# Performance work log

Hardware: AMD Instinct MI355X
Metric: run time of the kernel (lower is better)

## Reference

```python
import jax, jax.numpy as jnp
import numpy as np

B, T, C = 256, 256, 147
BPM, H_DIM, NH = 32, 64, 4
HD = H_DIM // NH


def setup_inputs() -> dict:
    key = jax.random.key(0)
    ks = jax.random.split(key, 12)
    def lin(k, fan_in, fan_out):
        bound = 1.0 / np.sqrt(fan_in)
        kw, kb = jax.random.split(k)
        W = jax.random.uniform(kw, (fan_in, fan_out), jnp.float32, -bound, bound)
        b = jax.random.uniform(kb, (fan_out,), jnp.float32, -bound, bound)
        return W, b
    Wq, bq = lin(ks[0], C, H_DIM)
    Wk, bk = lin(ks[1], C, H_DIM)
    Wv, bv = lin(ks[2], C, H_DIM)
    Wb, bb = lin(ks[3], BPM, H_DIM)
    Wo, bo = lin(ks[4], H_DIM, C)
    pose = jax.random.normal(ks[5], (B, T, C), jnp.float32)
    bpm_emb = jax.random.normal(ks[6], (B, BPM), jnp.float32)
    return {"pose": pose, "bpm_emb": bpm_emb,
            "Wq": Wq, "bq": bq, "Wk": Wk, "bk": bk, "Wv": Wv, "bv": bv,
            "Wb": Wb, "bb": bb, "Wo": Wo, "bo": bo}


def reference(pose, bpm_emb, Wq, bq, Wk, bk, Wv, bv, Wb, bb, Wo, bo):
    Bb, Tt, Cc = pose.shape
    scale = HD ** -0.5
    # projections -> [B, H, T, hd]
    def split_heads(x):
        return x.reshape(Bb, Tt, NH, HD).transpose(0, 2, 1, 3)
    q = split_heads(pose @ Wq + bq)
    k = split_heads(pose @ Wk + bk)
    v = split_heads(pose @ Wv + bv)
    # bpm-conditioned key bias: [B, H, 1, hd]
    bpm_feat = (bpm_emb @ Wb + bb).reshape(Bb, 1, NH, HD).transpose(0, 2, 1, 3)
    k = k + bpm_feat
    # attention
    scores = jnp.einsum('bhqd,bhkd->bhqk', q, k) * scale
    attn = jax.nn.softmax(scores, axis=-1)
    out = jnp.einsum('bhqk,bhkd->bhqd', attn, v)
    out = out.transpose(0, 2, 1, 3).reshape(Bb, Tt, NH * HD)
    return out @ Wo + bo
```

## Files before the change

### kernel.cpp

```cpp
#include <hip/hip_runtime.h>

constexpr int kC = 147, kH = 64, kBPM = 32;

typedef __attribute__((ext_vector_type(8)))  short bf16x8;
typedef __attribute__((ext_vector_type(4)))  float f32x4;
typedef __attribute__((ext_vector_type(16))) float f32x16;
typedef __attribute__((ext_vector_type(2)))  unsigned u32x2;
typedef __attribute__((ext_vector_type(4)))  unsigned u32x4;

__device__ __forceinline__ short f2bf(float f) {
    unsigned u = __builtin_bit_cast(unsigned, f);
    u += 0x7fffu + ((u >> 16) & 1u);
    return (short)(u >> 16);
}
__device__ __forceinline__ unsigned cvt_pk(float lo, float hi) {
    unsigned r;
    asm("v_cvt_pk_bf16_f32 %0, %1, %2" : "=v"(r) : "v"(lo), "v"(hi));
    return r;
}
#define MFMA16(a,b,c) __builtin_amdgcn_mfma_f32_16x16x32_bf16((a),(b),(c),0,0,0)
#define MFMA32(a,b,c) __builtin_amdgcn_mfma_f32_32x32x16_bf16((a),(b),(c),0,0,0)

#if __has_builtin(__builtin_amdgcn_exp2f)
  #define EXP2(x) __builtin_amdgcn_exp2f(x)
#else
  #define EXP2(x) __expf((x) * 0.6931471805599453f)
#endif
constexpr float kQScale = 0.25f * 1.4426950408889634f;

constexpr int QS  = 72;
constexpr int VS  = 264;
constexpr int WSS = 168;
constexpr int WOS = 72;

__device__ __forceinline__ void stage_w_regs(const float* wr ,
                                             short* Ws, int tid) {
    #pragma unroll
    for (int it = 0; it < 5; ++it) {
        const int i = it * 1024 + tid;
        const int c = i & 63, k = (i >> 6) * 2;
        *(unsigned*)&Ws[c * WSS + (k ^ (((c >> 3) & 3) << 3))]
            = cvt_pk(wr[2*it], wr[2*it + 1]);
    }
}

__global__ __launch_bounds__(1024, 4) void fused_kernel(
    const float* __restrict__ pose, const float* __restrict__ bpm_emb,
    const float* __restrict__ Wq, const float* __restrict__ bq,
    const float* __restrict__ Wk, const float* __restrict__ bk,
    const float* __restrict__ Wv, const float* __restrict__ bv,
    const float* __restrict__ Wb, const float* __restrict__ bb,
    const float* __restrict__ Wo, const float* __restrict__ bo,
    float* __restrict__ out)
{
    __shared__ __align__(16) short qs[256 * QS];
    __shared__ __align__(16) short ks_[256 * QS];
    __shared__ __align__(16) short vt[kH * VS];
    __shared__ __align__(16) short Ws[11520];
    __shared__ float bias_s[192];

    const int tid = threadIdx.x;
    const int w = tid >> 6, lane = tid & 63;
    const int ll = lane & 15, lq = lane >> 4;
    const int lm = lane & 31, lh = lane >> 5;
    const int b = blockIdx.x;
    const size_t pbase = (size_t)b * 256 * kC;

    float wq_r[10], wk_r[10], wv_r[10], wo_r[10];
    #pragma unroll
    for (int it = 0; it < 5; ++it) {
        const int i = it * 1024 + tid;
        const int c = i & 63, k = (i >> 6) * 2;
        const bool b0 = k < kC, b1 = k + 1 < kC;
        wq_r[2*it]   = b0 ? Wq[k * kH + c] * kQScale : 0.f;
        wq_r[2*it+1] = b1 ? Wq[(k + 1) * kH + c] * kQScale : 0.f;
        wk_r[2*it]   = b0 ? Wk[k * kH + c] : 0.f;
        wk_r[2*it+1] = b1 ? Wk[(k + 1) * kH + c] : 0.f;
        wv_r[2*it]   = b0 ? Wv[k * kH + c] : 0.f;
        wv_r[2*it+1] = b1 ? Wv[(k + 1) * kH + c] : 0.f;
        const int n = i % 160, ko = (i / 160) * 2;
        wo_r[2*it]   = (n < kC) ? Wo[ko * kC + n] : 0.f;
        wo_r[2*it+1] = (n < kC) ? Wo[(ko + 1) * kC + n] : 0.f;
    }

    bf16x8 pf[5];
    {
        const int row = w * 16 + ll;
        const float* prow = pose + pbase + (size_t)row * kC;
        #pragma unroll
        for (int ksp = 0; ksp < 5; ++ksp) {
            const int c0 = ksp * 32 + lq * 8;
            float v[8];
            if (c0 + 8 <= kC) {
                const float4 f0 = *(const float4*)(prow + c0);
                const float4 f1 = *(const float4*)(prow + c0 + 4);
                v[0]=f0.x; v[1]=f0.y; v[2]=f0.z; v[3]=f0.w;
                v[4]=f1.x; v[5]=f1.y; v[6]=f1.z; v[7]=f1.w;
            } else {
                #pragma unroll
                for (int e = 0; e < 8; ++e) v[e] = (c0 + e < kC) ? prow[c0 + e] : 0.f;
            }
            const u32x4 t = { cvt_pk(v[0], v[1]), cvt_pk(v[2], v[3]),
                              cvt_pk(v[4], v[5]), cvt_pk(v[6], v[7]) };
            pf[ksp] = __builtin_bit_cast(bf16x8, t);
        }
    }
    if (tid < 192) {
        const int m = tid >> 6, c = tid & 63;
        float a = ((m == 0) ? bq : (m == 1) ? bk : bv)[c];
        if (m == 1) {
            a += bb[c];
            #pragma unroll
            for (int k2 = 0; k2 < kBPM; ++k2)
                a = fmaf(bpm_emb[b * kBPM + k2], Wb[k2 * kH + c], a);
        }
        if (m == 0) a *= kQScale;
        bias_s[tid] = a;
    }
    stage_w_regs(wq_r, Ws, tid);
    __syncthreads();

    #pragma unroll
    for (int m = 0; m < 3; ++m) {
        f32x4 acc[4];
        #pragma unroll
        for (int mt = 0; mt < 4; ++mt) acc[mt] = (f32x4){0.f,0.f,0.f,0.f};
        #pragma unroll
        for (int ksp = 0; ksp < 5; ++ksp)
            #pragma unroll
            for (int mt = 0; mt < 4; ++mt) {
                const int c = mt * 16 + ll;
                const int key = ((c >> 3) & 3) << 3;
                const bf16x8 wf = *(const bf16x8*)(Ws + c * WSS + ((ksp*32 + lq*8) ^ key));
                acc[mt] = MFMA16(wf, pf[ksp], acc[mt]);
            }
        __syncthreads();
        if (m == 0)      stage_w_regs(wk_r, Ws, tid);
        else if (m == 1) stage_w_regs(wv_r, Ws, tid);
        else {
            #pragma unroll
            for (int it = 0; it < 5; ++it) {
                const int i = it * 1024 + tid;
                const int n = i % 160, k = (i / 160) * 2;
                *(unsigned*)&Ws[n * WOS + (k ^ (((n >> 3) & 3) << 3))]
                    = cvt_pk(wo_r[2*it], wo_r[2*it + 1]);
            }
        }
        const int row = w * 16 + ll;
        #pragma unroll
        for (int mt = 0; mt < 4; ++mt) {
            const int c0 = mt * 16 + 4 * lq;
            const float4 bv4 = *(const float4*)&bias_s[m * kH + c0];
            if (m < 2) {
                const u32x2 pk = { cvt_pk(acc[mt][0] + bv4.x, acc[mt][1] + bv4.y),
                                   cvt_pk(acc[mt][2] + bv4.z, acc[mt][3] + bv4.w) };
                *(u32x2*)((m == 0 ? qs : ks_) + row * QS + c0) = pk;
            } else {
                vt[(c0 + 0) * VS + row] = f2bf(acc[mt][0] + bv4.x);
                vt[(c0 + 1) * VS + row] = f2bf(acc[mt][1] + bv4.y);
                vt[(c0 + 2) * VS + row] = f2bf(acc[mt][2] + bv4.z);
                vt[(c0 + 3) * VS + row] = f2bf(acc[mt][3] + bv4.w);
            }
        }
        __syncthreads();
    }

    const int h = w & 3;
    const int q0 = (w >> 2) * 64;
    bf16x8 qf[2];
    #pragma unroll
    for (int s32 = 0; s32 < 2; ++s32)
        qf[s32] = *(const bf16x8*)(qs + (q0 + s32*32 + lm) * QS + h*16 + lh*8);

    f32x16 oacc[2];
    #pragma unroll
    for (int s32 = 0; s32 < 2; ++s32)
        oacc[s32] = (f32x16){0.f,0.f,0.f,0.f,0.f,0.f,0.f,0.f,
                             0.f,0.f,0.f,0.f,0.f,0.f,0.f,0.f};
    float lp[2] = {0.f, 0.f};
    const int vrow = h * 16 + (lm & 15);
    const f32x16 z16 = {0.f,0.f,0.f,0.f,0.f,0.f,0.f,0.f,
                        0.f,0.f,0.f,0.f,0.f,0.f,0.f,0.f};

    #pragma unroll 2
    for (int jb = 0; jb < 8; ++jb) {
        const int j0 = jb * 32;
        const bf16x8 kf  = *(const bf16x8*)(ks_ + (j0 + lm) * QS + h*16 + lh*8);
        const bf16x8 va0 = *(const bf16x8*)(vt + vrow * VS + j0 + lh*8);
        const bf16x8 va1 = *(const bf16x8*)(vt + vrow * VS + j0 + 16 + lh*8);
        #pragma unroll
        for (int s32 = 0; s32 < 2; ++s32) {
            const f32x16 s = MFMA32(kf, qf[s32], z16);
            float sum = 0.f;
            unsigned u[8];
            #pragma unroll
            for (int g = 0; g < 4; ++g) {
                const float p0 = EXP2(s[4*g + 0]);
                const float p1 = EXP2(s[4*g + 1]);
                const float p2 = EXP2(s[4*g + 2]);
                const float p3 = EXP2(s[4*g + 3]);
                sum += (p0 + p1) + (p2 + p3);
                u[2*g]   = cvt_pk(p0, p1);
                u[2*g+1] = cvt_pk(p2, p3);
            }
            lp[s32] += sum;
            unsigned a0 = u[0], a1 = u[1], b0 = u[2], b1 = u[3];
            asm("v_permlane32_swap_b32 %0, %1" : "+v"(a0), "+v"(b0));
            asm("v_permlane32_swap_b32 %0, %1" : "+v"(a1), "+v"(b1));
            unsigned c0 = u[4], c1 = u[5], d0 = u[6], d1 = u[7];
            asm("v_permlane32_swap_b32 %0, %1" : "+v"(c0), "+v"(d0));
            asm("v_permlane32_swap_b32 %0, %1" : "+v"(c1), "+v"(d1));
            const u32x4 pb0 = { a0, a1, b0, b1 };
            const u32x4 pb1 = { c0, c1, d0, d1 };
            oacc[s32] = MFMA32(va0, __builtin_bit_cast(bf16x8, pb0), oacc[s32]);
            oacc[s32] = MFMA32(va1, __builtin_bit_cast(bf16x8, pb1), oacc[s32]);
        }
    }
    #pragma unroll
    for (int s32 = 0; s32 < 2; ++s32) {
        const float l2 = lp[s32] + __shfl_xor(lp[s32], 32);
        const float inv = 1.f / l2;
        const int row = q0 + s32 * 32 + lm;
        const u32x2 pkA = { cvt_pk(oacc[s32][0] * inv, oacc[s32][1] * inv),
                            cvt_pk(oacc[s32][2] * inv, oacc[s32][3] * inv) };
        *(u32x2*)(qs + row * QS + h*16 + 4*lh) = pkA;
        const u32x2 pkB = { cvt_pk(oacc[s32][4] * inv, oacc[s32][5] * inv),
                            cvt_pk(oacc[s32][6] * inv, oacc[s32][7] * inv) };
        *(u32x2*)(qs + row * QS + h*16 + 8 + 4*lh) = pkB;
    }
    __syncthreads();

    bf16x8 xf[2];
    #pragma unroll
    for (int k2 = 0; k2 < 2; ++k2)
        xf[k2] = *(const bf16x8*)(qs + (w*16 + ll) * QS + k2*32 + lq*8);

    f32x4 po[10];
    #pragma unroll
    for (int mt = 0; mt < 10; ++mt) po[mt] = (f32x4){0.f,0.f,0.f,0.f};
    #pragma unroll
    for (int k2 = 0; k2 < 2; ++k2)
        #pragma unroll
        for (int mt = 0; mt < 10; ++mt) {
            const int n = mt * 16 + ll;
            const int key = ((n >> 3) & 3) << 3;
            const bf16x8 wf = *(const bf16x8*)(Ws + n * WOS + ((k2*32 + lq*8) ^ key));
            po[mt] = MFMA16(wf, xf[k2], po[mt]);
        }
    {
        const int row = w * 16 + ll;
        float* orow = out + ((size_t)b * 256 + row) * kC;
        #pragma unroll
        for (int mt = 0; mt < 10; ++mt) {
            const int c0 = mt * 16 + 4 * lq;
            if (mt < 9) {
                const float4 bv4 = *(const float4*)(bo + c0);
                float4 o;
                o.x = po[mt][0] + bv4.x; o.y = po[mt][1] + bv4.y;
                o.z = po[mt][2] + bv4.z; o.w = po[mt][3] + bv4.w;
                *(float4*)(orow + c0) = o;
            } else {
                #pragma unroll
                for (int r = 0; r < 4; ++r) {
                    const int c = c0 + r;
                    if (c < kC) orow[c] = po[mt][r] + bo[c];
                }
            }
        }
    }
}

extern "C" void kernel_launch(void* const* d_in, const int* in_sizes, int n_in,
                              void* d_out, int out_size, void* d_ws, size_t ws_size,
                              hipStream_t stream) {
    const float* pose    = (const float*)d_in[0];
    const float* bpm_emb = (const float*)d_in[1];
    const float* Wq = (const float*)d_in[2];  const float* bq = (const float*)d_in[3];
    const float* Wk = (const float*)d_in[4];  const float* bk = (const float*)d_in[5];
    const float* Wv = (const float*)d_in[6];  const float* bv = (const float*)d_in[7];
    const float* Wb = (const float*)d_in[8];  const float* bb = (const float*)d_in[9];
    const float* Wo = (const float*)d_in[10]; const float* bo = (const float*)d_in[11];
    float* out = (float*)d_out;

    fused_kernel<<<256, 1024, 0, stream>>>(
        pose, bpm_emb, Wq, bq, Wk, bk, Wv, bv, Wb, bb, Wo, bo, out);
}
```

Measured before the change: 132.0 us.

## Stage Q/K/V weights together, fuse projections, XOR-swizzle unpadded LDS tiles

Stages all three Q/K/V weight matrices into shared memory at once, so the three projections run in one MFMA loop with a single barrier instead of three staged rounds. The Q/K/V tiles drop their padding and use XOR swizzles to avoid bank conflicts. The Wo weight load is deferred until after the projections, which cuts live registers. The attention loop is restructured to process one 32-row query slice at a time, halving the accumulator registers. The cost is more LDS for the concurrently staged weights, which may reduce occupancy, and extra index arithmetic for the swizzles.

```diff
diff --git a/kernel.cpp b/kernel.cpp
--- a/kernel.cpp
+++ b/kernel.cpp
@@ -28,9 +28,7 @@
 #endif
 constexpr float kQScale = 0.25f * 1.4426950408889634f;
 
-constexpr int QS  = 72;
-constexpr int VS  = 264;
-constexpr int WSS = 168;
+constexpr int WSS = 160;
 constexpr int WOS = 72;
 
 __device__ __forceinline__ void stage_w_regs(const float* wr ,
@@ -53,11 +51,15 @@
     const float* __restrict__ Wo, const float* __restrict__ bo,
     float* __restrict__ out)
 {
-    __shared__ __align__(16) short qs[256 * QS];
-    __shared__ __align__(16) short ks_[256 * QS];
-    __shared__ __align__(16) short vt[kH * VS];
-    __shared__ __align__(16) short Ws[11520];
+    __shared__ __align__(16) short Wqkv[3 * 64 * WSS];
+    __shared__ __align__(16) short qs[256 * 64];
+    __shared__ __align__(16) short ks_[256 * 64];
+    __shared__ __align__(16) short vt[64 * 256];
     __shared__ float bias_s[192];
+    short* const Wqs = Wqkv;
+    short* const Wks = Wqkv + 64 * WSS;
+    short* const Wvs = Wqkv + 2 * 64 * WSS;
+    short* const Wos = Wqkv;
 
     const int tid = threadIdx.x;
     const int w = tid >> 6, lane = tid & 63;
@@ -65,23 +67,6 @@
     const int lm = lane & 31, lh = lane >> 5;
     const int b = blockIdx.x;
     const size_t pbase = (size_t)b * 256 * kC;
-
-    float wq_r[10], wk_r[10], wv_r[10], wo_r[10];
-    #pragma unroll
-    for (int it = 0; it < 5; ++it) {
-        const int i = it * 1024 + tid;
-        const int c = i & 63, k = (i >> 6) * 2;
-        const bool b0 = k < kC, b1 = k + 1 < kC;
-        wq_r[2*it]   = b0 ? Wq[k * kH + c] * kQScale : 0.f;
-        wq_r[2*it+1] = b1 ? Wq[(k + 1) * kH + c] * kQScale : 0.f;
-        wk_r[2*it]   = b0 ? Wk[k * kH + c] : 0.f;
-        wk_r[2*it+1] = b1 ? Wk[(k + 1) * kH + c] : 0.f;
-        wv_r[2*it]   = b0 ? Wv[k * kH + c] : 0.f;
-        wv_r[2*it+1] = b1 ? Wv[(k + 1) * kH + c] : 0.f;
-        const int n = i % 160, ko = (i / 160) * 2;
-        wo_r[2*it]   = (n < kC) ? Wo[ko * kC + n] : 0.f;
-        wo_r[2*it+1] = (n < kC) ? Wo[(ko + 1) * kC + n] : 0.f;
-    }
 
     bf16x8 pf[5];
     {
@@ -105,92 +90,115 @@
             pf[ksp] = __builtin_bit_cast(bf16x8, t);
         }
     }
-    if (tid < 192) {
-        const int m = tid >> 6, c = tid & 63;
-        float a = ((m == 0) ? bq : (m == 1) ? bk : bv)[c];
-        if (m == 1) {
-            a += bb[c];
-            #pragma unroll
-            for (int k2 = 0; k2 < kBPM; ++k2)
-                a = fmaf(bpm_emb[b * kBPM + k2], Wb[k2 * kH + c], a);
-        }
-        if (m == 0) a *= kQScale;
-        bias_s[tid] = a;
-    }
-    stage_w_regs(wq_r, Ws, tid);
+    {
+        float wq_r[10], wk_r[10], wv_r[10];
+        #pragma unroll
+        for (int it = 0; it < 5; ++it) {
+            const int i = it * 1024 + tid;
+            const int c = i & 63, k = (i >> 6) * 2;
+            const bool b0 = k < kC, b1 = k + 1 < kC;
+            wq_r[2*it]   = b0 ? Wq[k * kH + c] * kQScale : 0.f;
+            wq_r[2*it+1] = b1 ? Wq[(k + 1) * kH + c] * kQScale : 0.f;
+            wk_r[2*it]   = b0 ? Wk[k * kH + c] : 0.f;
+            wk_r[2*it+1] = b1 ? Wk[(k + 1) * kH + c] : 0.f;
+            wv_r[2*it]   = b0 ? Wv[k * kH + c] : 0.f;
+            wv_r[2*it+1] = b1 ? Wv[(k + 1) * kH + c] : 0.f;
+        }
+        if (tid < 192) {
+            const int m = tid >> 6, c = tid & 63;
+            float a = ((m == 0) ? bq : (m == 1) ? bk : bv)[c];
+            if (m == 1) {
+                a += bb[c];
+                #pragma unroll
+                for (int k2 = 0; k2 < kBPM; ++k2)
+                    a = fmaf(bpm_emb[b * kBPM + k2], Wb[k2 * kH + c], a);
+            }
+            if (m == 0) a *= kQScale;
+            bias_s[tid] = a;
+        }
+        stage_w_regs(wq_r, Wqs, tid);
+        stage_w_regs(wk_r, Wks, tid);
+        stage_w_regs(wv_r, Wvs, tid);
+    }
     __syncthreads();
 
-    #pragma unroll
-    for (int m = 0; m < 3; ++m) {
-        f32x4 acc[4];
-        #pragma unroll
-        for (int mt = 0; mt < 4; ++mt) acc[mt] = (f32x4){0.f,0.f,0.f,0.f};
-        #pragma unroll
-        for (int ksp = 0; ksp < 5; ++ksp)
-            #pragma unroll
-            for (int mt = 0; mt < 4; ++mt) {
-                const int c = mt * 16 + ll;
-                const int key = ((c >> 3) & 3) << 3;
-                const bf16x8 wf = *(const bf16x8*)(Ws + c * WSS + ((ksp*32 + lq*8) ^ key));
-                acc[mt] = MFMA16(wf, pf[ksp], acc[mt]);
-            }
-        __syncthreads();
-        if (m == 0)      stage_w_regs(wk_r, Ws, tid);
-        else if (m == 1) stage_w_regs(wv_r, Ws, tid);
-        else {
-            #pragma unroll
-            for (int it = 0; it < 5; ++it) {
-                const int i = it * 1024 + tid;
-                const int n = i % 160, k = (i / 160) * 2;
-                *(unsigned*)&Ws[n * WOS + (k ^ (((n >> 3) & 3) << 3))]
-                    = cvt_pk(wo_r[2*it], wo_r[2*it + 1]);
-            }
-        }
+    f32x4 aQ[4], aK[4], aV[4];
+    #pragma unroll
+    for (int mt = 0; mt < 4; ++mt) {
+        aQ[mt] = (f32x4){0.f,0.f,0.f,0.f};
+        aK[mt] = (f32x4){0.f,0.f,0.f,0.f};
+        aV[mt] = (f32x4){0.f,0.f,0.f,0.f};
+    }
+    #pragma unroll
+    for (int ksp = 0; ksp < 5; ++ksp)
+        #pragma unroll
+        for (int mt = 0; mt < 4; ++mt) {
+            const int c = mt * 16 + ll;
+            const int ko = (ksp*32 + lq*8) ^ (((c >> 3) & 3) << 3);
+            aQ[mt] = MFMA16(*(const bf16x8*)(Wqs + c * WSS + ko), pf[ksp], aQ[mt]);
+            aK[mt] = MFMA16(*(const bf16x8*)(Wks + c * WSS + ko), pf[ksp], aK[mt]);
+            aV[mt] = MFMA16(*(const bf16x8*)(Wvs + c * WSS + ko), pf[ksp], aV[mt]);
+        }
+    {
         const int row = w * 16 + ll;
+        const int rkey = (ll & 7) << 3;
         #pragma unroll
         for (int mt = 0; mt < 4; ++mt) {
             const int c0 = mt * 16 + 4 * lq;
-            const float4 bv4 = *(const float4*)&bias_s[m * kH + c0];
-            if (m < 2) {
-                const u32x2 pk = { cvt_pk(acc[mt][0] + bv4.x, acc[mt][1] + bv4.y),
-                                   cvt_pk(acc[mt][2] + bv4.z, acc[mt][3] + bv4.w) };
-                *(u32x2*)((m == 0 ? qs : ks_) + row * QS + c0) = pk;
-            } else {
-                vt[(c0 + 0) * VS + row] = f2bf(acc[mt][0] + bv4.x);
-                vt[(c0 + 1) * VS + row] = f2bf(acc[mt][1] + bv4.y);
-                vt[(c0 + 2) * VS + row] = f2bf(acc[mt][2] + bv4.z);
-                vt[(c0 + 3) * VS + row] = f2bf(acc[mt][3] + bv4.w);
-            }
-        }
-        __syncthreads();
+            const float4 bq4 = *(const float4*)&bias_s[0 * kH + c0];
+            const u32x2 pq = { cvt_pk(aQ[mt][0] + bq4.x, aQ[mt][1] + bq4.y),
+                               cvt_pk(aQ[mt][2] + bq4.z, aQ[mt][3] + bq4.w) };
+            *(u32x2*)(qs + row * 64 + (c0 ^ rkey)) = pq;
+            const float4 bk4 = *(const float4*)&bias_s[1 * kH + c0];
+            const u32x2 pk = { cvt_pk(aK[mt][0] + bk4.x, aK[mt][1] + bk4.y),
+                               cvt_pk(aK[mt][2] + bk4.z, aK[mt][3] + bk4.w) };
+            *(u32x2*)(ks_ + row * 64 + (c0 ^ rkey)) = pk;
+            const float4 bv4 = *(const float4*)&bias_s[2 * kH + c0];
+            vt[(c0 + 0) * 256 + (row ^ (((c0 + 0) & 7) << 3))] = f2bf(aV[mt][0] + bv4.x);
+            vt[(c0 + 1) * 256 + (row ^ (((c0 + 1) & 7) << 3))] = f2bf(aV[mt][1] + bv4.y);
+            vt[(c0 + 2) * 256 + (row ^ (((c0 + 2) & 7) << 3))] = f2bf(aV[mt][2] + bv4.z);
+            vt[(c0 + 3) * 256 + (row ^ (((c0 + 3) & 7) << 3))] = f2bf(aV[mt][3] + bv4.w);
+        }
+    }
+    float wo_r[10];
+    #pragma unroll
+    for (int it = 0; it < 5; ++it) {
+        const int i = it * 1024 + tid;
+        const int n = i % 160, k = (i / 160) * 2;
+        wo_r[2*it]   = (n < kC) ? Wo[k * kC + n] : 0.f;
+        wo_r[2*it+1] = (n < kC) ? Wo[(k + 1) * kC + n] : 0.f;
+    }
+    __syncthreads();
+
+    #pragma unroll
+    for (int it = 0; it < 5; ++it) {
+        const int i = it * 1024 + tid;
+        const int n = i % 160, k = (i / 160) * 2;
+        *(unsigned*)&Wos[n * WOS + (k ^ (((n >> 3) & 3) << 3))]
+            = cvt_pk(wo_r[2*it], wo_r[2*it + 1]);
     }
 
     const int h = w & 3;
     const int q0 = (w >> 2) * 64;
-    bf16x8 qf[2];
-    #pragma unroll
-    for (int s32 = 0; s32 < 2; ++s32)
-        qf[s32] = *(const bf16x8*)(qs + (q0 + s32*32 + lm) * QS + h*16 + lh*8);
-
-    f32x16 oacc[2];
-    #pragma unroll
-    for (int s32 = 0; s32 < 2; ++s32)
-        oacc[s32] = (f32x16){0.f,0.f,0.f,0.f,0.f,0.f,0.f,0.f,
-                             0.f,0.f,0.f,0.f,0.f,0.f,0.f,0.f};
-    float lp[2] = {0.f, 0.f};
     const int vrow = h * 16 + (lm & 15);
+    const int vkey = (vrow & 7) << 3;
+    const int ckey = (lm & 7) << 3;
     const f32x16 z16 = {0.f,0.f,0.f,0.f,0.f,0.f,0.f,0.f,
                         0.f,0.f,0.f,0.f,0.f,0.f,0.f,0.f};
 
-    #pragma unroll 2
-    for (int jb = 0; jb < 8; ++jb) {
-        const int j0 = jb * 32;
-        const bf16x8 kf  = *(const bf16x8*)(ks_ + (j0 + lm) * QS + h*16 + lh*8);
-        const bf16x8 va0 = *(const bf16x8*)(vt + vrow * VS + j0 + lh*8);
-        const bf16x8 va1 = *(const bf16x8*)(vt + vrow * VS + j0 + 16 + lh*8);
-        #pragma unroll
-        for (int s32 = 0; s32 < 2; ++s32) {
-            const f32x16 s = MFMA32(kf, qf[s32], z16);
+    #pragma unroll
+    for (int s32 = 0; s32 < 2; ++s32) {
+        const int qrow = q0 + s32 * 32 + lm;
+        const bf16x8 qf = *(const bf16x8*)(qs + qrow * 64 + ((h*16 + lh*8) ^ ckey));
+        f32x16 oacc = z16;
+        float lp = 0.f;
+        #pragma unroll 2
+        for (int jb = 0; jb < 8; ++jb) {
+            const int j0 = jb * 32;
+            const bf16x8 kf  = *(const bf16x8*)(ks_ + (j0 + lm) * 64 + ((h*16 + lh*8) ^ ckey));
+            const bf16x8 va0 = *(const bf16x8*)(vt + vrow * 256 + ((j0 + lh*8) ^ vkey));
+            const bf16x8 va1 = *(const bf16x8*)(vt + vrow * 256 + ((j0 + 16 + lh*8) ^ vkey));
+            const f32x16 s = MFMA32(kf, qf, z16);
             float sum = 0.f;
             unsigned u[8];
             #pragma unroll
@@ -203,7 +211,7 @@
                 u[2*g]   = cvt_pk(p0, p1);
                 u[2*g+1] = cvt_pk(p2, p3);
             }
-            lp[s32] += sum;
+            lp += sum;
             unsigned a0 = u[0], a1 = u[1], b0 = u[2], b1 = u[3];
             asm("v_permlane32_swap_b32 %0, %1" : "+v"(a0), "+v"(b0));
             asm("v_permlane32_swap_b32 %0, %1" : "+v"(a1), "+v"(b1));
@@ -212,28 +220,26 @@
             asm("v_permlane32_swap_b32 %0, %1" : "+v"(c1), "+v"(d1));
             const u32x4 pb0 = { a0, a1, b0, b1 };
             const u32x4 pb1 = { c0, c1, d0, d1 };
-            oacc[s32] = MFMA32(va0, __builtin_bit_cast(bf16x8, pb0), oacc[s32]);
-            oacc[s32] = MFMA32(va1, __builtin_bit_cast(bf16x8, pb1), oacc[s32]);
-        }
-    }
-    #pragma unroll
-    for (int s32 = 0; s32 < 2; ++s32) {
-        const float l2 = lp[s32] + __shfl_xor(lp[s32], 32);
+            oacc = MFMA32(va0, __builtin_bit_cast(bf16x8, pb0), oacc);
+            oacc = MFMA32(va1, __builtin_bit_cast(bf16x8, pb1), oacc);
+        }
+        const float l2 = lp + __shfl_xor(lp, 32);
         const float inv = 1.f / l2;
-        const int row = q0 + s32 * 32 + lm;
-        const u32x2 pkA = { cvt_pk(oacc[s32][0] * inv, oacc[s32][1] * inv),
-                            cvt_pk(oacc[s32][2] * inv, oacc[s32][3] * inv) };
-        *(u32x2*)(qs + row * QS + h*16 + 4*lh) = pkA;
-        const u32x2 pkB = { cvt_pk(oacc[s32][4] * inv, oacc[s32][5] * inv),
-                            cvt_pk(oacc[s32][6] * inv, oacc[s32][7] * inv) };
-        *(u32x2*)(qs + row * QS + h*16 + 8 + 4*lh) = pkB;
+        const u32x2 pkA = { cvt_pk(oacc[0] * inv, oacc[1] * inv),
+                            cvt_pk(oacc[2] * inv, oacc[3] * inv) };
+        *(u32x2*)(qs + qrow * 64 + ((h*16 + 4*lh) ^ ckey)) = pkA;
+        const u32x2 pkB = { cvt_pk(oacc[4] * inv, oacc[5] * inv),
+                            cvt_pk(oacc[6] * inv, oacc[7] * inv) };
+        *(u32x2*)(qs + qrow * 64 + ((h*16 + 8 + 4*lh) ^ ckey)) = pkB;
     }
     __syncthreads();
 
+    const int xr = w * 16 + ll;
+    const int xkey = (ll & 7) << 3;
     bf16x8 xf[2];
     #pragma unroll
     for (int k2 = 0; k2 < 2; ++k2)
-        xf[k2] = *(const bf16x8*)(qs + (w*16 + ll) * QS + k2*32 + lq*8);
+        xf[k2] = *(const bf16x8*)(qs + xr * 64 + ((k2*32 + lq*8) ^ xkey));
 
     f32x4 po[10];
     #pragma unroll
@@ -244,12 +250,11 @@
         for (int mt = 0; mt < 10; ++mt) {
             const int n = mt * 16 + ll;
             const int key = ((n >> 3) & 3) << 3;
-            const bf16x8 wf = *(const bf16x8*)(Ws + n * WOS + ((k2*32 + lq*8) ^ key));
+            const bf16x8 wf = *(const bf16x8*)(Wos + n * WOS + ((k2*32 + lq*8) ^ key));
             po[mt] = MFMA16(wf, xf[k2], po[mt]);
         }
     {
-        const int row = w * 16 + ll;
-        float* orow = out + ((size_t)b * 256 + row) * kC;
+        float* orow = out + ((size_t)b * 256 + xr) * kC;
         #pragma unroll
         for (int mt = 0; mt < 10; ++mt) {
             const int c0 = mt * 16 + 4 * lq;
```

Result: no change. 129.8 us (-1.6%).
